# Kernel optimization log

Hardware: AMD Instinct MI355X
Metric: run time of the kernel (lower is better)

The kernel has to match this reference:

```python
import jax, jax.numpy as jnp
import numpy as np

N, I, H = 32, 64, 128
B, T = 16, 256


def setup_inputs() -> dict:
    key = jax.random.key(0)
    k1, k2, k3, k4, k5 = jax.random.split(key, 5)
    stdv = 1.0 / np.sqrt(H)
    x = jax.random.normal(k1, (B, T, N * I), dtype=jnp.float32)
    h0 = jnp.zeros((1, B, N * H), dtype=jnp.float32)
    c0 = jnp.zeros((1, B, N * H), dtype=jnp.float32)
    # Block-diagonal weights stored as batched per-block matrices.
    # weight_ih block i is [4H, I], weight_hh block i is [4H, H].
    weight_ih = jax.random.uniform(k2, (N, 4 * H, I), jnp.float32, -stdv, stdv)
    weight_hh = jax.random.uniform(k3, (N, 4 * H, H), jnp.float32, -stdv, stdv)
    bias_ih = jax.random.uniform(k4, (N, 4 * H), jnp.float32, -stdv, stdv)
    bias_hh = jax.random.uniform(k5, (N, 4 * H), jnp.float32, -stdv, stdv)
    return {"x": x, "h0": h0, "c0": c0, "weight_ih": weight_ih,
            "weight_hh": weight_hh, "bias_ih": bias_ih, "bias_hh": bias_hh}


def _wide_lstm(x, h0, c0, weight_ih, weight_hh, bias_ih, bias_hh):
    b, t, _ = x.shape
    xb = x.reshape(b, t, N, I)
    # Precompute input-to-gate projections for all timesteps: [B,T,N,4H]
    gates_x = jnp.einsum('btni,ngi->btng', xb, weight_ih) + bias_ih
    h_t = h0[0].reshape(b, N, H)
    c_t = c0[0].reshape(b, N, H)

    def step(carry, gx_t):
        h, c = carry
        gates_h = jnp.einsum('bnh,ngh->bng', h, weight_hh) + bias_hh
        gates = gx_t + gates_h  # [B,N,4H]
        i_g = jax.nn.sigmoid(gates[..., 0 * H:1 * H])
        f_g = jax.nn.sigmoid(gates[..., 1 * H:2 * H])
        g_g = jnp.tanh(gates[..., 2 * H:3 * H])
        o_g = jax.nn.sigmoid(gates[..., 3 * H:4 * H])
        c_new = f_g * c + i_g * g_g
        h_new = o_g * jnp.tanh(c_new)
        return (h_new, c_new), h_new

    (h_n, c_n), outs = jax.lax.scan(step, (h_t, c_t),
                                    jnp.swapaxes(gates_x, 0, 1))  # scan over T
    output = jnp.swapaxes(outs, 0, 1).reshape(b, t, N * H)
    return output, h_n.reshape(1, b, N * H), c_n.reshape(1, b, N * H)


def reference(x, h0, c0, weight_ih, weight_hh, bias_ih, bias_hh):
    return _wide_lstm(x, h0, c0, weight_ih, weight_hh, bias_ih, bias_hh)
```

## Files before the change

kernel.cpp:

```cpp
#include <hip/hip_runtime.h>
#include <hip/hip_bf16.h>
#include <cstdint>
#include <cstddef>


#define TSTEPS 256

typedef float  f32x4  __attribute__((ext_vector_type(4)));
typedef float  f32x2  __attribute__((ext_vector_type(2)));
typedef __bf16 bf16x8 __attribute__((ext_vector_type(8)));
typedef short  s16x8  __attribute__((ext_vector_type(8)));

union Frag { s16x8 s; bf16x8 b; };

#define KSIG -1.4426950408889634f
#define KTAN  2.8853900817779268f

__device__ __forceinline__ short f2bf(float f) {
  uint32_t u = __builtin_bit_cast(uint32_t, f);
  u += 0x7fffu + ((u >> 16) & 1u);
  return (short)(u >> 16);
}

__device__ __forceinline__ void sync_lds() {
  asm volatile("s_waitcnt lgkmcnt(0)" ::: "memory");
  __builtin_amdgcn_s_barrier();
  asm volatile("" ::: "memory");
}

__device__ __forceinline__ float sig2(float z) {
  return __builtin_amdgcn_rcpf(1.f + __builtin_amdgcn_exp2f(z));
}

__device__ __forceinline__ f32x4 mf(const Frag a, const Frag bb, f32x4 c) {
  return __builtin_amdgcn_mfma_f32_16x16x32_bf16(a.b, bb.b, c, 0, 0, 0);
}

__global__ __launch_bounds__(512, 2) void wide_lstm(
    const float* __restrict__ x,   const float* __restrict__ h0,
    const float* __restrict__ c0,  const float* __restrict__ wih,
    const float* __restrict__ whh, const float* __restrict__ bih,
    const float* __restrict__ bhh, float* __restrict__ out)
{
  const int n    = blockIdx.x & 31;
  const int bg   = blockIdx.x >> 5;
  const int tid  = threadIdx.x;
  const int w    = tid >> 6;
  const int lane = tid & 63;
  const int col  = lane & 15;
  const int quad = lane >> 4;
  const int b4   = col & 3;
  const int e2   = col >> 2;
  const int hloc = 4 * quad + e2;
  const int hgl  = 16 * w + hloc;
  const int b    = 4 * bg + b4;

  __shared__ alignas(16) short hbuf[2][4 * 144];
  __shared__ alignas(16) short xbuf[2][4 * 96];

  Frag wfr[6][4];
#pragma unroll
  for (int j = 0; j < 4; ++j) {
    const int g = 128 * j + 16 * w + col;
#pragma unroll
    for (int s = 0; s < 6; ++s) {
      const int k0 = 32 * s + quad * 8;
      const float* p = (s < 2) ? (wih + (size_t)(n * 512 + g) * 64  + k0)
                               : (whh + (size_t)(n * 512 + g) * 128 + (k0 - 64));
      const f32x4 lo = *(const f32x4*)p;
      const f32x4 hi = *(const f32x4*)(p + 4);
      Frag f;
      f.s[0]=f2bf(lo[0]); f.s[1]=f2bf(lo[1]); f.s[2]=f2bf(lo[2]); f.s[3]=f2bf(lo[3]);
      f.s[4]=f2bf(hi[0]); f.s[5]=f2bf(hi[1]); f.s[6]=f2bf(hi[2]); f.s[7]=f2bf(hi[3]);
      wfr[s][j] = f;
    }
  }

  f32x4 cb[4];
#pragma unroll
  for (int j = 0; j < 4; ++j) {
    const int base = n * 512 + 128 * j + 16 * w + quad * 4;
    const f32x4 b1 = *(const f32x4*)(bih + base);
    const f32x4 b2 = *(const f32x4*)(bhh + base);
#pragma unroll
    for (int r = 0; r < 4; ++r) cb[j][r] = b1[r] + b2[r];
  }
  const f32x4 kzero = (f32x4){0.f, 0.f, 0.f, 0.f};

  if (tid < 256) {
    const int bi = tid >> 6, j2 = (tid & 63) * 2;
    const f32x2 hv = *(const f32x2*)(h0 + (size_t)(4 * bg + bi) * 4096 + n * 128 + j2);
    *(uint32_t*)&hbuf[0][bi * 144 + j2] =
        (uint32_t)(uint16_t)f2bf(hv[0]) | ((uint32_t)(uint16_t)f2bf(hv[1]) << 16);
  }
  const int bq = tid >> 6;
  const int kq = tid & 63;
  const float* xp = x + (size_t)(4 * bg + bq) * (TSTEPS * 2048) + n * 64 + kq;
  float xr = 0.f;
  if (tid < 256) {
    xbuf[1][bq * 96 + kq] = f2bf(xp[2048]);
    xr = xp[2 * 2048];
  }
  const float* xnext = xp + 3 * 2048;
  float cg = c0[(size_t)b * 4096 + n * 128 + hgl];

  f32x4 acpre[4];
  {
    const float* q = x + (size_t)b * (TSTEPS * 2048) + n * 64 + 8 * quad;
    const f32x4 a0 = *(const f32x4*)q;
    const f32x4 a1 = *(const f32x4*)(q + 4);
    const f32x4 a2 = *(const f32x4*)(q + 32);
    const f32x4 a3 = *(const f32x4*)(q + 36);
    Frag xf0, xf1;
#pragma unroll
    for (int r = 0; r < 4; ++r) {
      xf0.s[r]     = f2bf(a0[r]);
      xf0.s[4 + r] = f2bf(a1[r]);
      xf1.s[r]     = f2bf(a2[r]);
      xf1.s[4 + r] = f2bf(a3[r]);
    }
#pragma unroll
    for (int j = 0; j < 4; ++j)
      acpre[j] = mf(wfr[1][j], xf1, mf(wfr[0][j], xf0, cb[j]));
  }
  __syncthreads();

  const int xoff  = b4 * 96  + quad * 8;
  const int hoff  = b4 * 144 + quad * 8;
  const int sxoff = bq * 96 + kq;
  const int hwoff = b4 * 144 + hgl;
  float* outp = out + (size_t)b * (TSTEPS * 4096) + n * 128 + hgl;
  float ho = 0.f;
  const bool m1 = (e2 & 1), m2 = (e2 & 2);

#define LSTM_STEP(CUR, NXT, S)                                               \
  {                                                                          \
    Frag hf0, hf1, hf2, hf3;                                                 \
    hf0.s = *(const s16x8*)&hbuf[CUR][hoff];                                 \
    hf1.s = *(const s16x8*)&hbuf[CUR][hoff + 32];                            \
    hf2.s = *(const s16x8*)&hbuf[CUR][hoff + 64];                            \
    hf3.s = *(const s16x8*)&hbuf[CUR][hoff + 96];                            \
    if (tid < 256) {                                                         \
      xbuf[CUR][sxoff] = f2bf(xr);                                           \
      if ((S) + 3 < TSTEPS) { xr = *xnext; xnext += 2048; }                  \
    }                                                                        \
    f32x4 ac1[4], ac2[4];                                                    \
    _Pragma("unroll") for (int j = 0; j < 4; ++j) {                          \
      ac1[j] = mf(wfr[2][j], hf0, acpre[j]);                                 \
      ac2[j] = mf(wfr[4][j], hf2, kzero);                                    \
    }                                                                        \
    _Pragma("unroll") for (int j = 0; j < 4; ++j) {                          \
      ac1[j] = mf(wfr[3][j], hf1, ac1[j]);                                   \
      ac2[j] = mf(wfr[5][j], hf3, ac2[j]);                                   \
    }                                                                        \
    __builtin_amdgcn_sched_barrier(0);  \
    Frag xg0, xg1;                                                           \
    xg0.s = *(const s16x8*)&xbuf[NXT][xoff];                                 \
    xg1.s = *(const s16x8*)&xbuf[NXT][xoff + 32];                            \
    float pre[4];                                                            \
    _Pragma("unroll") for (int j = 0; j < 4; ++j) {                          \
      const float u01 = m1 ? ac1[j][1] : ac1[j][0];                          \
      const float u23 = m1 ? ac1[j][3] : ac1[j][2];                          \
      const float v01 = m1 ? ac2[j][1] : ac2[j][0];                          \
      const float v23 = m1 ? ac2[j][3] : ac2[j][2];                          \
      pre[j] = (m2 ? u23 : u01) + (m2 ? v23 : v01);                          \
    }                                                                        \
    const float si = sig2(KSIG * pre[0]);                                    \
    const float sf = sig2(KSIG * pre[1]);                                    \
    const float sg = sig2(KTAN * pre[2]);                                    \
    const float so = sig2(KSIG * pre[3]);                                    \
    float cn = __builtin_fmaf(sf, cg, si);                                   \
    cn = __builtin_fmaf(-2.f, si * sg, cn);                                  \
    cg = cn;                                                                 \
    ho = so * __builtin_fmaf(-2.f, sig2(KTAN * cn), 1.f);                    \
    _Pragma("unroll") for (int j = 0; j < 4; ++j)                            \
      acpre[j] = mf(wfr[0][j], xg0, cb[j]);                                  \
    _Pragma("unroll") for (int j = 0; j < 4; ++j)                            \
      acpre[j] = mf(wfr[1][j], xg1, acpre[j]);                               \
    hbuf[NXT][hwoff] = f2bf(ho);                                             \
    *outp = ho;                                                              \
    outp += 4096;                                                            \
    sync_lds();                                                              \
  }

  for (int t = 0; t < TSTEPS; t += 2) {
    LSTM_STEP(0, 1, t);
    LSTM_STEP(1, 0, t + 1);
  }
#undef LSTM_STEP

  out[16777216 +         (size_t)b * 4096 + n * 128 + hgl] = ho;
  out[16777216 + 65536 + (size_t)b * 4096 + n * 128 + hgl] = cg;
}

extern "C" void kernel_launch(void* const* d_in, const int* in_sizes, int n_in,
                              void* d_out, int out_size, void* d_ws, size_t ws_size,
                              hipStream_t stream) {
  const float* x   = (const float*)d_in[0];
  const float* h0  = (const float*)d_in[1];
  const float* c0  = (const float*)d_in[2];
  const float* wih = (const float*)d_in[3];
  const float* whh = (const float*)d_in[4];
  const float* bih = (const float*)d_in[5];
  const float* bhh = (const float*)d_in[6];
  float* out = (float*)d_out;
  wide_lstm<<<128, 512, 0, stream>>>(x, h0, c0, wih, whh, bih, bhh, out);
}
```

Measured before the change: 292.2 us.

## Split recurrent GEMM across two wave groups with LDS partial-sum exchange

Doubles the block to 1024 threads. Waves 0-7 handle the x projection, the first K-slice of the h GEMM and the gate math, while waves 8-15 compute the remaining three K-slices of h·Whh and pass partial sums through a new LDS buffer. The intent is to shorten the serial MFMA chain on the per-timestep critical path by running the K-reduction in parallel. The cost is an extra barrier per step, plus LDS round-trips for the partials, which may offset the shorter chain.

Result: faster. 267.9 us (-8.3%).

```diff
diff --git a/kernel.cpp b/kernel.cpp
--- a/kernel.cpp
+++ b/kernel.cpp
@@ -36,7 +36,13 @@
   return __builtin_amdgcn_mfma_f32_16x16x32_bf16(a.b, bb.b, c, 0, 0, 0);
 }
 
-__global__ __launch_bounds__(512, 2) void wide_lstm(
+__device__ __forceinline__ float sel4(const f32x4 a, bool m1, bool m2) {
+  const float u01 = m1 ? a[1] : a[0];
+  const float u23 = m1 ? a[3] : a[2];
+  return m2 ? u23 : u01;
+}
+
+__global__ __launch_bounds__(1024, 4) void wide_lstm(
     const float* __restrict__ x,   const float* __restrict__ h0,
     const float* __restrict__ c0,  const float* __restrict__ wih,
     const float* __restrict__ whh, const float* __restrict__ bih,
@@ -45,7 +51,9 @@
   const int n    = blockIdx.x & 31;
   const int bg   = blockIdx.x >> 5;
   const int tid  = threadIdx.x;
-  const int w    = tid >> 6;
+  const int wv   = tid >> 6;
+  const int w    = wv & 7;
+  const bool isw = (wv < 8);
   const int lane = tid & 63;
   const int col  = lane & 15;
   const int quad = lane >> 4;
@@ -57,13 +65,15 @@
 
   __shared__ alignas(16) short hbuf[2][4 * 144];
   __shared__ alignas(16) short xbuf[2][4 * 96];
-
-  Frag wfr[6][4];
+  __shared__ alignas(16) float pbuf[8][64][4];
+
+  Frag wfr[3][4];
 #pragma unroll
   for (int j = 0; j < 4; ++j) {
     const int g = 128 * j + 16 * w + col;
 #pragma unroll
-    for (int s = 0; s < 6; ++s) {
+    for (int sl = 0; sl < 3; ++sl) {
+      const int s = isw ? sl : sl + 3;
       const int k0 = 32 * s + quad * 8;
       const float* p = (s < 2) ? (wih + (size_t)(n * 512 + g) * 64  + k0)
                                : (whh + (size_t)(n * 512 + g) * 128 + (k0 - 64));
@@ -72,99 +82,81 @@
       Frag f;
       f.s[0]=f2bf(lo[0]); f.s[1]=f2bf(lo[1]); f.s[2]=f2bf(lo[2]); f.s[3]=f2bf(lo[3]);
       f.s[4]=f2bf(hi[0]); f.s[5]=f2bf(hi[1]); f.s[6]=f2bf(hi[2]); f.s[7]=f2bf(hi[3]);
-      wfr[s][j] = f;
-    }
-  }
-
-  f32x4 cb[4];
-#pragma unroll
-  for (int j = 0; j < 4; ++j) {
-    const int base = n * 512 + 128 * j + 16 * w + quad * 4;
-    const f32x4 b1 = *(const f32x4*)(bih + base);
-    const f32x4 b2 = *(const f32x4*)(bhh + base);
-#pragma unroll
-    for (int r = 0; r < 4; ++r) cb[j][r] = b1[r] + b2[r];
-  }
+      wfr[sl][j] = f;
+    }
+  }
+
+  const int hoff  = b4 * 144 + quad * 8;
+  const int hwoff = b4 * 144 + hgl;
+  const int xoff  = b4 * 96  + quad * 8;
+  const bool m1 = (e2 & 1), m2 = (e2 & 2);
   const f32x4 kzero = (f32x4){0.f, 0.f, 0.f, 0.f};
 
-  if (tid < 256) {
-    const int bi = tid >> 6, j2 = (tid & 63) * 2;
-    const f32x2 hv = *(const f32x2*)(h0 + (size_t)(4 * bg + bi) * 4096 + n * 128 + j2);
-    *(uint32_t*)&hbuf[0][bi * 144 + j2] =
-        (uint32_t)(uint16_t)f2bf(hv[0]) | ((uint32_t)(uint16_t)f2bf(hv[1]) << 16);
-  }
-  const int bq = tid >> 6;
-  const int kq = tid & 63;
-  const float* xp = x + (size_t)(4 * bg + bq) * (TSTEPS * 2048) + n * 64 + kq;
+  f32x4 cb[4], acpre[4];
+  float cg = 0.f, ho = 0.f;
+  float* outp = nullptr;
   float xr = 0.f;
-  if (tid < 256) {
+  const float* xnext = nullptr;
+
+  if (isw) {
+#pragma unroll
+    for (int j = 0; j < 4; ++j) {
+      const int base = n * 512 + 128 * j + 16 * w + quad * 4;
+      const f32x4 b1 = *(const f32x4*)(bih + base);
+      const f32x4 b2 = *(const f32x4*)(bhh + base);
+#pragma unroll
+      for (int r = 0; r < 4; ++r) cb[j][r] = b1[r] + b2[r];
+    }
+    if (tid < 256) {
+      const int bi = tid >> 6, j2 = (tid & 63) * 2;
+      const f32x2 hv = *(const f32x2*)(h0 + (size_t)(4 * bg + bi) * 4096 + n * 128 + j2);
+      *(uint32_t*)&hbuf[0][bi * 144 + j2] =
+          (uint32_t)(uint16_t)f2bf(hv[0]) | ((uint32_t)(uint16_t)f2bf(hv[1]) << 16);
+    }
+    cg = c0[(size_t)b * 4096 + n * 128 + hgl];
+    {
+      const float* q = x + (size_t)b * (TSTEPS * 2048) + n * 64 + 8 * quad;
+      const f32x4 a0 = *(const f32x4*)q;
+      const f32x4 a1 = *(const f32x4*)(q + 4);
+      const f32x4 a2 = *(const f32x4*)(q + 32);
+      const f32x4 a3 = *(const f32x4*)(q + 36);
+      Frag xf0, xf1;
+#pragma unroll
+      for (int r = 0; r < 4; ++r) {
+        xf0.s[r]     = f2bf(a0[r]);
+        xf0.s[4 + r] = f2bf(a1[r]);
+        xf1.s[r]     = f2bf(a2[r]);
+        xf1.s[4 + r] = f2bf(a3[r]);
+      }
+#pragma unroll
+      for (int j = 0; j < 4; ++j)
+        acpre[j] = mf(wfr[1][j], xf1, mf(wfr[0][j], xf0, cb[j]));
+    }
+    outp = out + (size_t)b * (TSTEPS * 4096) + n * 128 + hgl;
+  } else if (tid < 768) {
+    const int bq = (tid >> 6) & 3;
+    const int kq = tid & 63;
+    const float* xp = x + (size_t)(4 * bg + bq) * (TSTEPS * 2048) + n * 64 + kq;
     xbuf[1][bq * 96 + kq] = f2bf(xp[2048]);
     xr = xp[2 * 2048];
-  }
-  const float* xnext = xp + 3 * 2048;
-  float cg = c0[(size_t)b * 4096 + n * 128 + hgl];
-
-  f32x4 acpre[4];
-  {
-    const float* q = x + (size_t)b * (TSTEPS * 2048) + n * 64 + 8 * quad;
-    const f32x4 a0 = *(const f32x4*)q;
-    const f32x4 a1 = *(const f32x4*)(q + 4);
-    const f32x4 a2 = *(const f32x4*)(q + 32);
-    const f32x4 a3 = *(const f32x4*)(q + 36);
-    Frag xf0, xf1;
-#pragma unroll
-    for (int r = 0; r < 4; ++r) {
-      xf0.s[r]     = f2bf(a0[r]);
-      xf0.s[4 + r] = f2bf(a1[r]);
-      xf1.s[r]     = f2bf(a2[r]);
-      xf1.s[4 + r] = f2bf(a3[r]);
-    }
-#pragma unroll
-    for (int j = 0; j < 4; ++j)
-      acpre[j] = mf(wfr[1][j], xf1, mf(wfr[0][j], xf0, cb[j]));
+    xnext = xp + 3 * 2048;
   }
   __syncthreads();
 
-  const int xoff  = b4 * 96  + quad * 8;
-  const int hoff  = b4 * 144 + quad * 8;
-  const int sxoff = bq * 96 + kq;
-  const int hwoff = b4 * 144 + hgl;
-  float* outp = out + (size_t)b * (TSTEPS * 4096) + n * 128 + hgl;
-  float ho = 0.f;
-  const bool m1 = (e2 & 1), m2 = (e2 & 2);
-
-#define LSTM_STEP(CUR, NXT, S)                                               \
+  if (isw) {
+#define WSTEP(CUR, NXT, S)                                                   \
   {                                                                          \
-    Frag hf0, hf1, hf2, hf3;                                                 \
+    Frag hf0;                                                                \
     hf0.s = *(const s16x8*)&hbuf[CUR][hoff];                                 \
-    hf1.s = *(const s16x8*)&hbuf[CUR][hoff + 32];                            \
-    hf2.s = *(const s16x8*)&hbuf[CUR][hoff + 64];                            \
-    hf3.s = *(const s16x8*)&hbuf[CUR][hoff + 96];                            \
-    if (tid < 256) {                                                         \
-      xbuf[CUR][sxoff] = f2bf(xr);                                           \
-      if ((S) + 3 < TSTEPS) { xr = *xnext; xnext += 2048; }                  \
-    }                                                                        \
-    f32x4 ac1[4], ac2[4];                                                    \
-    _Pragma("unroll") for (int j = 0; j < 4; ++j) {                          \
+    f32x4 ac1[4];                                                            \
+    _Pragma("unroll") for (int j = 0; j < 4; ++j)                            \
       ac1[j] = mf(wfr[2][j], hf0, acpre[j]);                                 \
-      ac2[j] = mf(wfr[4][j], hf2, kzero);                                    \
-    }                                                                        \
-    _Pragma("unroll") for (int j = 0; j < 4; ++j) {                          \
-      ac1[j] = mf(wfr[3][j], hf1, ac1[j]);                                   \
-      ac2[j] = mf(wfr[5][j], hf3, ac2[j]);                                   \
-    }                                                                        \
-    __builtin_amdgcn_sched_barrier(0);  \
-    Frag xg0, xg1;                                                           \
-    xg0.s = *(const s16x8*)&xbuf[NXT][xoff];                                 \
-    xg1.s = *(const s16x8*)&xbuf[NXT][xoff + 32];                            \
     float pre[4];                                                            \
-    _Pragma("unroll") for (int j = 0; j < 4; ++j) {                          \
-      const float u01 = m1 ? ac1[j][1] : ac1[j][0];                          \
-      const float u23 = m1 ? ac1[j][3] : ac1[j][2];                          \
-      const float v01 = m1 ? ac2[j][1] : ac2[j][0];                          \
-      const float v23 = m1 ? ac2[j][3] : ac2[j][2];                          \
-      pre[j] = (m2 ? u23 : u01) + (m2 ? v23 : v01);                          \
-    }                                                                        \
+    _Pragma("unroll") for (int j = 0; j < 4; ++j)                            \
+      pre[j] = sel4(ac1[j], m1, m2);                                         \
+    sync_lds();                               \
+    const f32x4 vv = *(const f32x4*)&pbuf[w][lane][0];                       \
+    pre[0] += vv[0]; pre[1] += vv[1]; pre[2] += vv[2]; pre[3] += vv[3];      \
     const float si = sig2(KSIG * pre[0]);                                    \
     const float sf = sig2(KSIG * pre[1]);                                    \
     const float sg = sig2(KTAN * pre[2]);                                    \
@@ -173,24 +165,60 @@
     cn = __builtin_fmaf(-2.f, si * sg, cn);                                  \
     cg = cn;                                                                 \
     ho = so * __builtin_fmaf(-2.f, sig2(KTAN * cn), 1.f);                    \
-    _Pragma("unroll") for (int j = 0; j < 4; ++j)                            \
-      acpre[j] = mf(wfr[0][j], xg0, cb[j]);                                  \
-    _Pragma("unroll") for (int j = 0; j < 4; ++j)                            \
-      acpre[j] = mf(wfr[1][j], xg1, acpre[j]);                               \
     hbuf[NXT][hwoff] = f2bf(ho);                                             \
     *outp = ho;                                                              \
     outp += 4096;                                                            \
-    sync_lds();                                                              \
-  }
-
-  for (int t = 0; t < TSTEPS; t += 2) {
-    LSTM_STEP(0, 1, t);
-    LSTM_STEP(1, 0, t + 1);
-  }
-#undef LSTM_STEP
-
-  out[16777216 +         (size_t)b * 4096 + n * 128 + hgl] = ho;
-  out[16777216 + 65536 + (size_t)b * 4096 + n * 128 + hgl] = cg;
+    Frag xg0, xg1;                                                           \
+    xg0.s = *(const s16x8*)&xbuf[NXT][xoff];                                 \
+    xg1.s = *(const s16x8*)&xbuf[NXT][xoff + 32];                            \
+    _Pragma("unroll") for (int j = 0; j < 4; ++j)                            \
+      acpre[j] = mf(wfr[0][j], xg0, cb[j]);                                  \
+    _Pragma("unroll") for (int j = 0; j < 4; ++j)                            \
+      acpre[j] = mf(wfr[1][j], xg1, acpre[j]);                               \
+    sync_lds();                                                      \
+  }
+    for (int t = 0; t < TSTEPS; t += 2) {
+      WSTEP(0, 1, t);
+      WSTEP(1, 0, t + 1);
+    }
+#undef WSTEP
+    out[16777216 +         (size_t)b * 4096 + n * 128 + hgl] = ho;
+    out[16777216 + 65536 + (size_t)b * 4096 + n * 128 + hgl] = cg;
+  } else {
+    const int sxoff = ((tid >> 6) & 3) * 96 + (tid & 63);
+    const bool stg = (tid < 768);
+#define VSTEP(CUR, NXT, S)                                                   \
+  {                                                                          \
+    Frag hf1, hf2, hf3;                                                      \
+    hf1.s = *(const s16x8*)&hbuf[CUR][hoff + 32];                            \
+    hf2.s = *(const s16x8*)&hbuf[CUR][hoff + 64];                            \
+    hf3.s = *(const s16x8*)&hbuf[CUR][hoff + 96];                            \
+    if (stg) {                                                               \
+      xbuf[CUR][sxoff] = f2bf(xr);                                           \
+      if ((S) + 3 < TSTEPS) { xr = *xnext; xnext += 2048; }                  \
+    }                                                                        \
+    f32x4 ac[4];                                                             \
+    _Pragma("unroll") for (int j = 0; j < 4; ++j)                            \
+      ac[j] = mf(wfr[0][j], hf1, kzero);                                     \
+    _Pragma("unroll") for (int j = 0; j < 4; ++j)                            \
+      ac[j] = mf(wfr[1][j], hf2, ac[j]);                                     \
+    _Pragma("unroll") for (int j = 0; j < 4; ++j)                            \
+      ac[j] = mf(wfr[2][j], hf3, ac[j]);                                     \
+    f32x4 vv;                                                                \
+    vv[0] = sel4(ac[0], m1, m2);                                             \
+    vv[1] = sel4(ac[1], m1, m2);                                             \
+    vv[2] = sel4(ac[2], m1, m2);                                             \
+    vv[3] = sel4(ac[3], m1, m2);                                             \
+    *(f32x4*)&pbuf[w][lane][0] = vv;                                         \
+    sync_lds();                                                       \
+    sync_lds();                                                      \
+  }
+    for (int t = 0; t < TSTEPS; t += 2) {
+      VSTEP(0, 1, t);
+      VSTEP(1, 0, t + 1);
+    }
+#undef VSTEP
+  }
 }
 
 extern "C" void kernel_launch(void* const* d_in, const int* in_sizes, int n_in,
@@ -204,5 +232,5 @@
   const float* bih = (const float*)d_in[5];
   const float* bhh = (const float*)d_in[6];
   float* out = (float*)d_out;
-  wide_lstm<<<128, 512, 0, stream>>>(x, h0, c0, wih, whh, bih, bhh, out);
-}
+  wide_lstm<<<128, 1024, 0, stream>>>(x, h0, c0, wih, whh, bih, bhh, out);
+}
```

## Split gate work across 16 waves with gate-interleaved weight rows

Applied to the files above, without the earlier changes.

Doubles the block to 1024 threads (16 waves), so each wave owns 8 hidden units and holds half as many weight fragments and MFMAs per step. Weight rows are reordered so that each MFMA output column carries all four gates (i,f,g,o) for one hidden unit. This removes the per-lane select/shuffle that gathered gate preactivations, and the two 4-row tiles are selected with a single vector add. Half the lanes end up doing redundant gate math and skip their writes. The change cuts per-wave serial MFMA latency on the recurrent critical path, at the cost of a larger barrier across twice as many waves.

Result: slower. 301.8 us (+3.3%).

```diff
diff --git a/kernel.cpp b/kernel.cpp
--- a/kernel.cpp
+++ b/kernel.cpp
@@ -36,32 +36,34 @@
   return __builtin_amdgcn_mfma_f32_16x16x32_bf16(a.b, bb.b, c, 0, 0, 0);
 }
 
-__global__ __launch_bounds__(512, 2) void wide_lstm(
+__global__ __launch_bounds__(1024, 4) void wide_lstm(
     const float* __restrict__ x,   const float* __restrict__ h0,
     const float* __restrict__ c0,  const float* __restrict__ wih,
     const float* __restrict__ whh, const float* __restrict__ bih,
     const float* __restrict__ bhh, float* __restrict__ out)
 {
-  const int n    = blockIdx.x & 31;
-  const int bg   = blockIdx.x >> 5;
-  const int tid  = threadIdx.x;
-  const int w    = tid >> 6;
-  const int lane = tid & 63;
-  const int col  = lane & 15;
-  const int quad = lane >> 4;
-  const int b4   = col & 3;
-  const int e2   = col >> 2;
-  const int hloc = 4 * quad + e2;
-  const int hgl  = 16 * w + hloc;
-  const int b    = 4 * bg + b4;
+  const int n     = blockIdx.x & 31;
+  const int bg    = blockIdx.x >> 5;
+  const int tid   = threadIdx.x;
+  const int wv    = tid >> 6;
+  const int lane  = tid & 63;
+  const int col   = lane & 15;
+  const int quad  = lane >> 4;
+  const int b4    = col & 3;
+  const int e2    = col >> 2;
+  const int tsel  = e2 >> 1;
+  const int hbase = 8 * wv;
+  const int hl    = hbase + quad + 4 * tsel;
+  const int b     = 4 * bg + b4;
+  const bool wr   = ((e2 & 1) == 0);
 
   __shared__ alignas(16) short hbuf[2][4 * 144];
   __shared__ alignas(16) short xbuf[2][4 * 96];
 
-  Frag wfr[6][4];
+  Frag wfr[6][2];
 #pragma unroll
-  for (int j = 0; j < 4; ++j) {
-    const int g = 128 * j + 16 * w + col;
+  for (int T = 0; T < 2; ++T) {
+    const int g = 128 * (col & 3) + hbase + 4 * T + (col >> 2);
 #pragma unroll
     for (int s = 0; s < 6; ++s) {
       const int k0 = 32 * s + quad * 8;
@@ -72,20 +74,19 @@
       Frag f;
       f.s[0]=f2bf(lo[0]); f.s[1]=f2bf(lo[1]); f.s[2]=f2bf(lo[2]); f.s[3]=f2bf(lo[3]);
       f.s[4]=f2bf(hi[0]); f.s[5]=f2bf(hi[1]); f.s[6]=f2bf(hi[2]); f.s[7]=f2bf(hi[3]);
-      wfr[s][j] = f;
+      wfr[s][T] = f;
     }
   }
 
-  f32x4 cb[4];
+  f32x4 cb[2];
 #pragma unroll
-  for (int j = 0; j < 4; ++j) {
-    const int base = n * 512 + 128 * j + 16 * w + quad * 4;
-    const f32x4 b1 = *(const f32x4*)(bih + base);
-    const f32x4 b2 = *(const f32x4*)(bhh + base);
+  for (int T = 0; T < 2; ++T) {
 #pragma unroll
-    for (int r = 0; r < 4; ++r) cb[j][r] = b1[r] + b2[r];
+    for (int r = 0; r < 4; ++r) {
+      const int g = n * 512 + 128 * r + hbase + 4 * T + quad;
+      cb[T][r] = bih[g] + bhh[g];
+    }
   }
-  const f32x4 kzero = (f32x4){0.f, 0.f, 0.f, 0.f};
 
   if (tid < 256) {
     const int bi = tid >> 6, j2 = (tid & 63) * 2;
@@ -93,18 +94,19 @@
     *(uint32_t*)&hbuf[0][bi * 144 + j2] =
         (uint32_t)(uint16_t)f2bf(hv[0]) | ((uint32_t)(uint16_t)f2bf(hv[1]) << 16);
   }
-  const int bq = tid >> 6;
-  const int kq = tid & 63;
-  const float* xp = x + (size_t)(4 * bg + bq) * (TSTEPS * 2048) + n * 64 + kq;
+  const int sxoff = ((tid >> 6) & 3) * 96 + (tid & 63);
   float xr = 0.f;
+  const float* xnext = nullptr;
   if (tid < 256) {
+    const int bq = tid >> 6, kq = tid & 63;
+    const float* xp = x + (size_t)(4 * bg + bq) * (TSTEPS * 2048) + n * 64 + kq;
     xbuf[1][bq * 96 + kq] = f2bf(xp[2048]);
     xr = xp[2 * 2048];
+    xnext = xp + 3 * 2048;
   }
-  const float* xnext = xp + 3 * 2048;
-  float cg = c0[(size_t)b * 4096 + n * 128 + hgl];
+  float cg = c0[(size_t)b * 4096 + n * 128 + hl];
 
-  f32x4 acpre[4];
+  f32x4 acpre[2];
   {
     const float* q = x + (size_t)b * (TSTEPS * 2048) + n * 64 + 8 * quad;
     const f32x4 a0 = *(const f32x4*)q;
@@ -120,65 +122,51 @@
       xf1.s[4 + r] = f2bf(a3[r]);
     }
 #pragma unroll
-    for (int j = 0; j < 4; ++j)
-      acpre[j] = mf(wfr[1][j], xf1, mf(wfr[0][j], xf0, cb[j]));
+    for (int T = 0; T < 2; ++T)
+      acpre[T] = mf(wfr[1][T], xf1, mf(wfr[0][T], xf0, cb[T]));
   }
   __syncthreads();
 
+  const int hoff  = b4 * 144 + quad * 8;
   const int xoff  = b4 * 96  + quad * 8;
-  const int hoff  = b4 * 144 + quad * 8;
-  const int sxoff = bq * 96 + kq;
-  const int hwoff = b4 * 144 + hgl;
-  float* outp = out + (size_t)b * (TSTEPS * 4096) + n * 128 + hgl;
+  const int hwoff = b4 * 144 + hl;
+  float* outp = out + (size_t)b * (TSTEPS * 4096) + n * 128 + hl;
   float ho = 0.f;
-  const bool m1 = (e2 & 1), m2 = (e2 & 2);
+  const f32x4 kzero = (f32x4){0.f, 0.f, 0.f, 0.f};
 
 #define LSTM_STEP(CUR, NXT, S)                                               \
   {                                                                          \
-    Frag hf0, hf1, hf2, hf3;                                                 \
+    Frag hf0, hf1, hf2, hf3, xg0, xg1;                                       \
     hf0.s = *(const s16x8*)&hbuf[CUR][hoff];                                 \
     hf1.s = *(const s16x8*)&hbuf[CUR][hoff + 32];                            \
     hf2.s = *(const s16x8*)&hbuf[CUR][hoff + 64];                            \
     hf3.s = *(const s16x8*)&hbuf[CUR][hoff + 96];                            \
+    xg0.s = *(const s16x8*)&xbuf[NXT][xoff];                                 \
+    xg1.s = *(const s16x8*)&xbuf[NXT][xoff + 32];                            \
     if (tid < 256) {                                                         \
       xbuf[CUR][sxoff] = f2bf(xr);                                           \
       if ((S) + 3 < TSTEPS) { xr = *xnext; xnext += 2048; }                  \
     }                                                                        \
-    f32x4 ac1[4], ac2[4];                                                    \
-    _Pragma("unroll") for (int j = 0; j < 4; ++j) {                          \
-      ac1[j] = mf(wfr[2][j], hf0, acpre[j]);                                 \
-      ac2[j] = mf(wfr[4][j], hf2, kzero);                                    \
+    f32x4 ac1[2], ac2[2];                                                    \
+    _Pragma("unroll") for (int T = 0; T < 2; ++T) {                          \
+      ac1[T] = mf(wfr[3][T], hf1, mf(wfr[2][T], hf0, acpre[T]));             \
+      ac2[T] = mf(wfr[5][T], hf3, mf(wfr[4][T], hf2, kzero));                \
     }                                                                        \
-    _Pragma("unroll") for (int j = 0; j < 4; ++j) {                          \
-      ac1[j] = mf(wfr[3][j], hf1, ac1[j]);                                   \
-      ac2[j] = mf(wfr[5][j], hf3, ac2[j]);                                   \
-    }                                                                        \
-    __builtin_amdgcn_sched_barrier(0);  \
-    Frag xg0, xg1;                                                           \
-    xg0.s = *(const s16x8*)&xbuf[NXT][xoff];                                 \
-    xg1.s = *(const s16x8*)&xbuf[NXT][xoff + 32];                            \
-    float pre[4];                                                            \
-    _Pragma("unroll") for (int j = 0; j < 4; ++j) {                          \
-      const float u01 = m1 ? ac1[j][1] : ac1[j][0];                          \
-      const float u23 = m1 ? ac1[j][3] : ac1[j][2];                          \
-      const float v01 = m1 ? ac2[j][1] : ac2[j][0];                          \
-      const float v23 = m1 ? ac2[j][3] : ac2[j][2];                          \
-      pre[j] = (m2 ? u23 : u01) + (m2 ? v23 : v01);                          \
-    }                                                                        \
-    const float si = sig2(KSIG * pre[0]);                                    \
-    const float sf = sig2(KSIG * pre[1]);                                    \
-    const float sg = sig2(KTAN * pre[2]);                                    \
-    const float so = sig2(KSIG * pre[3]);                                    \
+    _Pragma("unroll") for (int T = 0; T < 2; ++T)                            \
+      acpre[T] = mf(wfr[1][T], xg1, mf(wfr[0][T], xg0, cb[T]));              \
+    const f32x4 ps = tsel ? (ac1[1] + ac2[1]) : (ac1[0] + ac2[0]);           \
+    const float si = sig2(KSIG * ps[0]);                                     \
+    const float sf = sig2(KSIG * ps[1]);                                     \
+    const float sg = sig2(KTAN * ps[2]);                                     \
+    const float so = sig2(KSIG * ps[3]);                                     \
     float cn = __builtin_fmaf(sf, cg, si);                                   \
     cn = __builtin_fmaf(-2.f, si * sg, cn);                                  \
     cg = cn;                                                                 \
     ho = so * __builtin_fmaf(-2.f, sig2(KTAN * cn), 1.f);                    \
-    _Pragma("unroll") for (int j = 0; j < 4; ++j)                            \
-      acpre[j] = mf(wfr[0][j], xg0, cb[j]);                                  \
-    _Pragma("unroll") for (int j = 0; j < 4; ++j)                            \
-      acpre[j] = mf(wfr[1][j], xg1, acpre[j]);                               \
-    hbuf[NXT][hwoff] = f2bf(ho);                                             \
-    *outp = ho;                                                              \
+    if (wr) {                                                                \
+      hbuf[NXT][hwoff] = f2bf(ho);                                           \
+      *outp = ho;                                                            \
+    }                                                                        \
     outp += 4096;                                                            \
     sync_lds();                                                              \
   }
@@ -189,8 +177,10 @@
   }
 #undef LSTM_STEP
 
-  out[16777216 +         (size_t)b * 4096 + n * 128 + hgl] = ho;
-  out[16777216 + 65536 + (size_t)b * 4096 + n * 128 + hgl] = cg;
+  if (wr) {
+    out[16777216 +         (size_t)b * 4096 + n * 128 + hl] = ho;
+    out[16777216 + 65536 + (size_t)b * 4096 + n * 128 + hl] = cg;
+  }
 }
 
 extern "C" void kernel_launch(void* const* d_in, const int* in_sizes, int n_in,
@@ -204,5 +194,5 @@
   const float* bih = (const float*)d_in[5];
   const float* bhh = (const float*)d_in[6];
   float* out = (float*)d_out;
-  wide_lstm<<<128, 512, 0, stream>>>(x, h0, c0, wih, whh, bih, bhh, out);
+  wide_lstm<<<128, 1024, 0, stream>>>(x, h0, c0, wih, whh, bih, bhh, out);
 }
```

## Split input projection onto dedicated helper waves feeding recurrence via LDS

Applied to the files above, without the earlier changes.

The block grows from 8 to 12 waves. Four helper waves compute the input-to-gate projection for the next timestep and write the selected gate pre-activations into a double-buffered LDS array. The 8 recurrence waves now run only the hidden-state MFMAs plus a single LDS read. This takes the x-projection MFMAs and the global x loads off the serial critical path, at the cost of more threads per block, an extra LDS buffer, and the helper waves joining every per-step barrier.

Result: faster. 281.7 us (-3.6%).

```diff
diff --git a/kernel.cpp b/kernel.cpp
--- a/kernel.cpp
+++ b/kernel.cpp
@@ -36,7 +36,13 @@
   return __builtin_amdgcn_mfma_f32_16x16x32_bf16(a.b, bb.b, c, 0, 0, 0);
 }
 
-__global__ __launch_bounds__(512, 2) void wide_lstm(
+__device__ __forceinline__ float sel4(const f32x4 a, bool m1, bool m2) {
+  const float u01 = m1 ? a[1] : a[0];
+  const float u23 = m1 ? a[3] : a[2];
+  return m2 ? u23 : u01;
+}
+
+__global__ __launch_bounds__(768, 2) void wide_lstm(
     const float* __restrict__ x,   const float* __restrict__ h0,
     const float* __restrict__ c0,  const float* __restrict__ wih,
     const float* __restrict__ whh, const float* __restrict__ bih,
@@ -45,7 +51,10 @@
   const int n    = blockIdx.x & 31;
   const int bg   = blockIdx.x >> 5;
   const int tid  = threadIdx.x;
-  const int w    = tid >> 6;
+  const int wv   = tid >> 6;
+  const bool isw = (wv < 8);
+  const int w    = wv & 7;
+  const int hw   = wv - 8;
   const int lane = tid & 63;
   const int col  = lane & 15;
   const int quad = lane >> 4;
@@ -57,114 +66,70 @@
 
   __shared__ alignas(16) short hbuf[2][4 * 144];
   __shared__ alignas(16) short xbuf[2][4 * 96];
-
-  Frag wfr[6][4];
-#pragma unroll
-  for (int j = 0; j < 4; ++j) {
-    const int g = 128 * j + 16 * w + col;
-#pragma unroll
-    for (int s = 0; s < 6; ++s) {
-      const int k0 = 32 * s + quad * 8;
-      const float* p = (s < 2) ? (wih + (size_t)(n * 512 + g) * 64  + k0)
-                               : (whh + (size_t)(n * 512 + g) * 128 + (k0 - 64));
-      const f32x4 lo = *(const f32x4*)p;
-      const f32x4 hi = *(const f32x4*)(p + 4);
-      Frag f;
-      f.s[0]=f2bf(lo[0]); f.s[1]=f2bf(lo[1]); f.s[2]=f2bf(lo[2]); f.s[3]=f2bf(lo[3]);
-      f.s[4]=f2bf(hi[0]); f.s[5]=f2bf(hi[1]); f.s[6]=f2bf(hi[2]); f.s[7]=f2bf(hi[3]);
-      wfr[s][j] = f;
-    }
-  }
-
-  f32x4 cb[4];
-#pragma unroll
-  for (int j = 0; j < 4; ++j) {
-    const int base = n * 512 + 128 * j + 16 * w + quad * 4;
-    const f32x4 b1 = *(const f32x4*)(bih + base);
-    const f32x4 b2 = *(const f32x4*)(bhh + base);
-#pragma unroll
-    for (int r = 0; r < 4; ++r) cb[j][r] = b1[r] + b2[r];
-  }
+  __shared__ alignas(16) float pbuf[2][8][64][4];
+
+  const int hoff  = b4 * 144 + quad * 8;
+  const int hwoff = b4 * 144 + hgl;
+  const int xoff  = b4 * 96  + quad * 8;
+  const bool m1 = (e2 & 1), m2 = (e2 & 2);
   const f32x4 kzero = (f32x4){0.f, 0.f, 0.f, 0.f};
 
-  if (tid < 256) {
-    const int bi = tid >> 6, j2 = (tid & 63) * 2;
-    const f32x2 hv = *(const f32x2*)(h0 + (size_t)(4 * bg + bi) * 4096 + n * 128 + j2);
-    *(uint32_t*)&hbuf[0][bi * 144 + j2] =
-        (uint32_t)(uint16_t)f2bf(hv[0]) | ((uint32_t)(uint16_t)f2bf(hv[1]) << 16);
-  }
-  const int bq = tid >> 6;
-  const int kq = tid & 63;
-  const float* xp = x + (size_t)(4 * bg + bq) * (TSTEPS * 2048) + n * 64 + kq;
-  float xr = 0.f;
-  if (tid < 256) {
-    xbuf[1][bq * 96 + kq] = f2bf(xp[2048]);
-    xr = xp[2 * 2048];
-  }
-  const float* xnext = xp + 3 * 2048;
-  float cg = c0[(size_t)b * 4096 + n * 128 + hgl];
-
-  f32x4 acpre[4];
-  {
-    const float* q = x + (size_t)b * (TSTEPS * 2048) + n * 64 + 8 * quad;
-    const f32x4 a0 = *(const f32x4*)q;
-    const f32x4 a1 = *(const f32x4*)(q + 4);
-    const f32x4 a2 = *(const f32x4*)(q + 32);
-    const f32x4 a3 = *(const f32x4*)(q + 36);
-    Frag xf0, xf1;
-#pragma unroll
-    for (int r = 0; r < 4; ++r) {
-      xf0.s[r]     = f2bf(a0[r]);
-      xf0.s[4 + r] = f2bf(a1[r]);
-      xf1.s[r]     = f2bf(a2[r]);
-      xf1.s[4 + r] = f2bf(a3[r]);
-    }
-#pragma unroll
-    for (int j = 0; j < 4; ++j)
-      acpre[j] = mf(wfr[1][j], xf1, mf(wfr[0][j], xf0, cb[j]));
-  }
-  __syncthreads();
-
-  const int xoff  = b4 * 96  + quad * 8;
-  const int hoff  = b4 * 144 + quad * 8;
-  const int sxoff = bq * 96 + kq;
-  const int hwoff = b4 * 144 + hgl;
-  float* outp = out + (size_t)b * (TSTEPS * 4096) + n * 128 + hgl;
-  float ho = 0.f;
-  const bool m1 = (e2 & 1), m2 = (e2 & 2);
-
-#define LSTM_STEP(CUR, NXT, S)                                               \
+  if (isw) {
+    Frag wfr[4][4];
+#pragma unroll
+    for (int j = 0; j < 4; ++j) {
+      const int g = 128 * j + 16 * w + col;
+#pragma unroll
+      for (int sl = 0; sl < 4; ++sl) {
+        const float* p = whh + (size_t)(n * 512 + g) * 128 + 32 * sl + quad * 8;
+        const f32x4 lo = *(const f32x4*)p;
+        const f32x4 hi = *(const f32x4*)(p + 4);
+        Frag f;
+        f.s[0]=f2bf(lo[0]); f.s[1]=f2bf(lo[1]); f.s[2]=f2bf(lo[2]); f.s[3]=f2bf(lo[3]);
+        f.s[4]=f2bf(hi[0]); f.s[5]=f2bf(hi[1]); f.s[6]=f2bf(hi[2]); f.s[7]=f2bf(hi[3]);
+        wfr[sl][j] = f;
+      }
+    }
+    f32x4 cb[4];
+#pragma unroll
+    for (int j = 0; j < 4; ++j) {
+      const int base = n * 512 + 128 * j + 16 * w + quad * 4;
+      const f32x4 b1 = *(const f32x4*)(bih + base);
+      const f32x4 b2 = *(const f32x4*)(bhh + base);
+#pragma unroll
+      for (int r = 0; r < 4; ++r) cb[j][r] = b1[r] + b2[r];
+    }
+    if (tid < 256) {
+      const int bi = tid >> 6, j2 = (tid & 63) * 2;
+      const f32x2 hv = *(const f32x2*)(h0 + (size_t)(4 * bg + bi) * 4096 + n * 128 + j2);
+      *(uint32_t*)&hbuf[0][bi * 144 + j2] =
+          (uint32_t)(uint16_t)f2bf(hv[0]) | ((uint32_t)(uint16_t)f2bf(hv[1]) << 16);
+    }
+    float cg = c0[(size_t)b * 4096 + n * 128 + hgl];
+    float* outp = out + (size_t)b * (TSTEPS * 4096) + n * 128 + hgl;
+    float ho = 0.f;
+    __syncthreads();
+
+#define CSTEP(P, Q, S)                                                       \
   {                                                                          \
     Frag hf0, hf1, hf2, hf3;                                                 \
-    hf0.s = *(const s16x8*)&hbuf[CUR][hoff];                                 \
-    hf1.s = *(const s16x8*)&hbuf[CUR][hoff + 32];                            \
-    hf2.s = *(const s16x8*)&hbuf[CUR][hoff + 64];                            \
-    hf3.s = *(const s16x8*)&hbuf[CUR][hoff + 96];                            \
-    if (tid < 256) {                                                         \
-      xbuf[CUR][sxoff] = f2bf(xr);                                           \
-      if ((S) + 3 < TSTEPS) { xr = *xnext; xnext += 2048; }                  \
-    }                                                                        \
+    hf0.s = *(const s16x8*)&hbuf[P][hoff];                                   \
+    hf1.s = *(const s16x8*)&hbuf[P][hoff + 32];                              \
+    hf2.s = *(const s16x8*)&hbuf[P][hoff + 64];                              \
+    hf3.s = *(const s16x8*)&hbuf[P][hoff + 96];                              \
+    const f32x4 xp4 = *(const f32x4*)&pbuf[P][w][lane][0];                   \
     f32x4 ac1[4], ac2[4];                                                    \
     _Pragma("unroll") for (int j = 0; j < 4; ++j) {                          \
-      ac1[j] = mf(wfr[2][j], hf0, acpre[j]);                                 \
-      ac2[j] = mf(wfr[4][j], hf2, kzero);                                    \
+      ac1[j] = mf(wfr[0][j], hf0, cb[j]);                                    \
+      ac2[j] = mf(wfr[2][j], hf2, kzero);                                    \
     }                                                                        \
     _Pragma("unroll") for (int j = 0; j < 4; ++j) {                          \
-      ac1[j] = mf(wfr[3][j], hf1, ac1[j]);                                   \
-      ac2[j] = mf(wfr[5][j], hf3, ac2[j]);                                   \
+      ac1[j] = mf(wfr[1][j], hf1, ac1[j]);                                   \
+      ac2[j] = mf(wfr[3][j], hf3, ac2[j]);                                   \
     }                                                                        \
-    __builtin_amdgcn_sched_barrier(0);  \
-    Frag xg0, xg1;                                                           \
-    xg0.s = *(const s16x8*)&xbuf[NXT][xoff];                                 \
-    xg1.s = *(const s16x8*)&xbuf[NXT][xoff + 32];                            \
     float pre[4];                                                            \
-    _Pragma("unroll") for (int j = 0; j < 4; ++j) {                          \
-      const float u01 = m1 ? ac1[j][1] : ac1[j][0];                          \
-      const float u23 = m1 ? ac1[j][3] : ac1[j][2];                          \
-      const float v01 = m1 ? ac2[j][1] : ac2[j][0];                          \
-      const float v23 = m1 ? ac2[j][3] : ac2[j][2];                          \
-      pre[j] = (m2 ? u23 : u01) + (m2 ? v23 : v01);                          \
-    }                                                                        \
+    _Pragma("unroll") for (int j = 0; j < 4; ++j)                            \
+      pre[j] = sel4(ac1[j], m1, m2) + sel4(ac2[j], m1, m2) + xp4[j];         \
     const float si = sig2(KSIG * pre[0]);                                    \
     const float sf = sig2(KSIG * pre[1]);                                    \
     const float sg = sig2(KTAN * pre[2]);                                    \
@@ -173,24 +138,98 @@
     cn = __builtin_fmaf(-2.f, si * sg, cn);                                  \
     cg = cn;                                                                 \
     ho = so * __builtin_fmaf(-2.f, sig2(KTAN * cn), 1.f);                    \
-    _Pragma("unroll") for (int j = 0; j < 4; ++j)                            \
-      acpre[j] = mf(wfr[0][j], xg0, cb[j]);                                  \
-    _Pragma("unroll") for (int j = 0; j < 4; ++j)                            \
-      acpre[j] = mf(wfr[1][j], xg1, acpre[j]);                               \
-    hbuf[NXT][hwoff] = f2bf(ho);                                             \
+    hbuf[Q][hwoff] = f2bf(ho);                                               \
     *outp = ho;                                                              \
     outp += 4096;                                                            \
     sync_lds();                                                              \
   }
-
-  for (int t = 0; t < TSTEPS; t += 2) {
-    LSTM_STEP(0, 1, t);
-    LSTM_STEP(1, 0, t + 1);
+    for (int t = 0; t < TSTEPS; t += 2) {
+      CSTEP(0, 1, t);
+      CSTEP(1, 0, t + 1);
+    }
+#undef CSTEP
+    out[16777216 +         (size_t)b * 4096 + n * 128 + hgl] = ho;
+    out[16777216 + 65536 + (size_t)b * 4096 + n * 128 + hgl] = cg;
+
+  } else {
+    Frag wfx[2][2][4];
+#pragma unroll
+    for (int T2 = 0; T2 < 2; ++T2) {
+      const int wt = 2 * hw + T2;
+#pragma unroll
+      for (int j = 0; j < 4; ++j) {
+        const int g = 128 * j + 16 * wt + col;
+#pragma unroll
+        for (int s = 0; s < 2; ++s) {
+          const float* p = wih + (size_t)(n * 512 + g) * 64 + 32 * s + quad * 8;
+          const f32x4 lo = *(const f32x4*)p;
+          const f32x4 hi = *(const f32x4*)(p + 4);
+          Frag f;
+          f.s[0]=f2bf(lo[0]); f.s[1]=f2bf(lo[1]); f.s[2]=f2bf(lo[2]); f.s[3]=f2bf(lo[3]);
+          f.s[4]=f2bf(hi[0]); f.s[5]=f2bf(hi[1]); f.s[6]=f2bf(hi[2]); f.s[7]=f2bf(hi[3]);
+          wfx[T2][s][j] = f;
+        }
+      }
+    }
+    const int sxoff = hw * 96 + lane;
+    const float* xp = x + (size_t)(4 * bg + hw) * (TSTEPS * 2048) + n * 64 + lane;
+    xbuf[1][sxoff] = f2bf(xp[2048]);
+    float xr = xp[2 * 2048];
+    const float* xnext = xp + 3 * 2048;
+    {
+      const float* q = x + (size_t)b * (TSTEPS * 2048) + n * 64 + 8 * quad;
+      const f32x4 a0 = *(const f32x4*)q;
+      const f32x4 a1 = *(const f32x4*)(q + 4);
+      const f32x4 a2 = *(const f32x4*)(q + 32);
+      const f32x4 a3 = *(const f32x4*)(q + 36);
+      Frag xf0, xf1;
+#pragma unroll
+      for (int r = 0; r < 4; ++r) {
+        xf0.s[r]     = f2bf(a0[r]);
+        xf0.s[4 + r] = f2bf(a1[r]);
+        xf1.s[r]     = f2bf(a2[r]);
+        xf1.s[4 + r] = f2bf(a3[r]);
+      }
+#pragma unroll
+      for (int T2 = 0; T2 < 2; ++T2) {
+        f32x4 acc[4];
+#pragma unroll
+        for (int j = 0; j < 4; ++j)
+          acc[j] = mf(wfx[T2][1][j], xf1, mf(wfx[T2][0][j], xf0, kzero));
+        f32x4 vv;
+        vv[0] = sel4(acc[0], m1, m2); vv[1] = sel4(acc[1], m1, m2);
+        vv[2] = sel4(acc[2], m1, m2); vv[3] = sel4(acc[3], m1, m2);
+        *(f32x4*)&pbuf[0][2 * hw + T2][lane][0] = vv;
+      }
+    }
+    __syncthreads();
+
+#define HSTEP(P, Q, S)                                                       \
+  {                                                                          \
+    Frag xg0, xg1;                                                           \
+    xg0.s = *(const s16x8*)&xbuf[Q][xoff];                                   \
+    xg1.s = *(const s16x8*)&xbuf[Q][xoff + 32];                              \
+    xbuf[P][sxoff] = f2bf(xr);                                               \
+    if ((S) + 3 < TSTEPS) { xr = *xnext; xnext += 2048; }                    \
+    _Pragma("unroll") for (int T2 = 0; T2 < 2; ++T2) {                       \
+      f32x4 acc[4];                                                          \
+      _Pragma("unroll") for (int j = 0; j < 4; ++j)                          \
+        acc[j] = mf(wfx[T2][0][j], xg0, kzero);                              \
+      _Pragma("unroll") for (int j = 0; j < 4; ++j)                          \
+        acc[j] = mf(wfx[T2][1][j], xg1, acc[j]);                             \
+      f32x4 vv;                                                              \
+      vv[0] = sel4(acc[0], m1, m2); vv[1] = sel4(acc[1], m1, m2);            \
+      vv[2] = sel4(acc[2], m1, m2); vv[3] = sel4(acc[3], m1, m2);            \
+      *(f32x4*)&pbuf[Q][2 * hw + T2][lane][0] = vv;                          \
+    }                                                                        \
+    sync_lds();                                                              \
   }
-#undef LSTM_STEP
-
-  out[16777216 +         (size_t)b * 4096 + n * 128 + hgl] = ho;
-  out[16777216 + 65536 + (size_t)b * 4096 + n * 128 + hgl] = cg;
+    for (int t = 0; t < TSTEPS; t += 2) {
+      HSTEP(0, 1, t);
+      HSTEP(1, 0, t + 1);
+    }
+#undef HSTEP
+  }
 }
 
 extern "C" void kernel_launch(void* const* d_in, const int* in_sizes, int n_in,
@@ -204,5 +243,5 @@
   const float* bih = (const float*)d_in[5];
   const float* bhh = (const float*)d_in[6];
   float* out = (float*)d_out;
-  wide_lstm<<<128, 512, 0, stream>>>(x, h0, c0, wih, whh, bih, bhh, out);
-}
+  wide_lstm<<<128, 768, 0, stream>>>(x, h0, c0, wih, whh, bih, bhh, out);
+}
```
